# Kernel optimization log

Hardware: AMD Instinct MI355X
Metric: run time of the kernel (lower is better)

## Reference

```python
import jax, jax.numpy as jnp
import numpy as np
import math

H = 16          # num_heads
EPS = 1e-5      # LayerNorm eps (torch default)


def setup_inputs() -> dict:
    key = jax.random.key(0)
    ks = jax.random.split(key, 4)
    B, T, D = 2, 2048, 1024
    s = 1.0 / math.sqrt(D)
    return {
        "x": jax.random.normal(ks[0], (B, T, D), dtype=jnp.float32),
        "ln_g": jnp.ones((D,), jnp.float32),
        "ln_b": jnp.zeros((D,), jnp.float32),
        "Wq": jax.random.normal(ks[1], (D, D), jnp.float32) * s,
        "bq": jnp.zeros((D,), jnp.float32),
        "Wk": jax.random.normal(ks[2], (D, D), jnp.float32) * s,
        "bk": jnp.zeros((D,), jnp.float32),
        "Wv": jax.random.normal(ks[3], (D, D), jnp.float32) * s,
        "bv": jnp.zeros((D,), jnp.float32),
    }


def reference(x, ln_g, ln_b, Wq, bq, Wk, bk, Wv, bv):
    B, T, D = x.shape
    # LayerNorm (shared across the three projections, computed once)
    mu = jnp.mean(x, axis=-1, keepdims=True)
    var = jnp.mean(jnp.square(x - mu), axis=-1, keepdims=True)
    xn = (x - mu) * jax.lax.rsqrt(var + EPS) * ln_g + ln_b
    # Q/K/V projections -> [B, T, H, Dh]
    q = (xn @ Wq + bq).reshape(B, T, H, D // H)
    k = (xn @ Wk + bk).reshape(B, T, H, D // H)
    v = (xn @ Wv + bv).reshape(B, T, H, D // H)
    # QK^T scores [B, n, m, h], scaled by sqrt(head_dim)
    scale = 1.0 / math.sqrt(D // H)
    attn = jnp.einsum('bnhd,bmhd->bnmh', q, k) * scale
    # softmax over key axis (dim=2), dropout p=0 is identity
    w = jax.nn.softmax(attn, axis=2)
    # weighted sum of values, merge heads
    y = jnp.einsum('bnmh,bmhd->bnhd', w, v).reshape(B, T, D)
    return y
```

## Files before the change

### kernel.cpp

```cpp
#include <hip/hip_runtime.h>
#include <hip/hip_bf16.h>


typedef __attribute__((ext_vector_type(8)))  short short8;
typedef __attribute__((ext_vector_type(4)))  float f32x4;
typedef __attribute__((ext_vector_type(2)))  float f32x2;
typedef __attribute__((ext_vector_type(16))) float f32x16;
typedef __attribute__((ext_vector_type(2)))  unsigned int uint2v;

#define D_MODEL 1024
#define T_SEQ   2048
#define NHEAD   16
#define HDIM    64

#define LOG2E 1.4426950408889634f

#if defined(__has_builtin)
#if __has_builtin(__builtin_amdgcn_exp2f)
#define EXP2(x) __builtin_amdgcn_exp2f(x)
#endif
#if __has_builtin(__builtin_amdgcn_permlane32_swap)
#define HAVE_PERMSWAP 1
#endif
#endif
#ifndef EXP2
#define EXP2(x) exp2f(x)
#endif

__device__ __forceinline__ unsigned short f2bf(float x) {
    unsigned int u = __float_as_uint(x);
    u = (u + 0x7fffu + ((u >> 16) & 1u)) >> 16;
    return (unsigned short)u;
}

__device__ __forceinline__ uint2v permswap(unsigned a, unsigned b) {
#ifdef HAVE_PERMSWAP
    return __builtin_amdgcn_permlane32_swap(a, b, false, false);
#else
    uint2v r;
    const unsigned as = (unsigned)__shfl_xor((int)a, 32, 64);
    const unsigned bs = (unsigned)__shfl_xor((int)b, 32, 64);
    const bool hi = (threadIdx.x & 32) != 0;
    r[0] = hi ? bs : a;
    r[1] = hi ? b  : as;
    return r;
#endif
}

__device__ __forceinline__ void group_barrier() {
    asm volatile("s_waitcnt lgkmcnt(0)" ::: "memory");
    __builtin_amdgcn_s_barrier();
    asm volatile("" ::: "memory");
}

__device__ __forceinline__ void w8(unsigned short* p, const uint4 v) {
    uint2 a; a.x = v.x; a.y = v.y;
    uint2 b; b.x = v.z; b.y = v.w;
    *(uint2*)p = a;
    *(uint2*)(p + 4) = b;
}

__device__ __forceinline__ short8 read8(const unsigned short* p) {
    union { unsigned u[4]; short8 s; } r;
    const uint2 a = *(const uint2*)p;
    const uint2 b = *(const uint2*)(p + 4);
    r.u[0] = a.x; r.u[1] = a.y; r.u[2] = b.x; r.u[3] = b.y;
    return r.s;
}

__global__ __launch_bounds__(256) void ln_wcast_kernel(
    const float* __restrict__ x, const float* __restrict__ gam,
    const float* __restrict__ bet, unsigned short* __restrict__ xn,
    const float* __restrict__ Wq, const float* __restrict__ Wk,
    const float* __restrict__ Wv, unsigned short* __restrict__ Wt)
{
    __shared__ float red[8];
    __shared__ float tile[32][33];
    const int bid = blockIdx.x;
    if (bid < 4096) {
        const int row = bid;
        const int t = threadIdx.x;
        const float4 v = ((const float4*)(x + (size_t)row * D_MODEL))[t];
        float s  = v.x + v.y + v.z + v.w;
        float s2 = v.x * v.x + v.y * v.y + v.z * v.z + v.w * v.w;
#pragma unroll
        for (int off = 32; off; off >>= 1) {
            s  += __shfl_down(s,  off, 64);
            s2 += __shfl_down(s2, off, 64);
        }
        const int lane = t & 63, wave = t >> 6;
        if (lane == 0) { red[wave] = s; red[4 + wave] = s2; }
        __syncthreads();
        s  = red[0] + red[1] + red[2] + red[3];
        s2 = red[4] + red[5] + red[6] + red[7];
        const float mu   = s * (1.f / D_MODEL);
        const float var  = s2 * (1.f / D_MODEL) - mu * mu;
        const float rstd = rsqrtf(var + 1e-5f);
        const float4 gv = ((const float4*)gam)[t];
        const float4 bv = ((const float4*)bet)[t];
        ushort4 o;
        o.x = f2bf((v.x - mu) * rstd * gv.x + bv.x);
        o.y = f2bf((v.y - mu) * rstd * gv.y + bv.y);
        o.z = f2bf((v.z - mu) * rstd * gv.z + bv.z);
        o.w = f2bf((v.w - mu) * rstd * gv.w + bv.w);
        ((ushort4*)(xn + (size_t)row * D_MODEL))[t] = o;
    } else {
        const int id = bid - 4096;
        const int z  = id >> 10;
        const int t2 = id & 1023;
        const int n0 = (t2 & 31) * 32, k0 = (t2 >> 5) * 32;
        const float* W = (z == 0) ? Wq : (z == 1) ? Wk : Wv;
        unsigned short* outw = Wt + (size_t)z * D_MODEL * D_MODEL;
        const int tx = threadIdx.x & 31, ty = threadIdx.x >> 5;
#pragma unroll
        for (int i = ty; i < 32; i += 8)
            tile[i][tx] = W[(size_t)(k0 + i) * D_MODEL + n0 + tx];
        __syncthreads();
#pragma unroll
        for (int i = ty; i < 32; i += 8)
            outw[(size_t)(n0 + i) * D_MODEL + k0 + tx] = f2bf(tile[tx][i]);
    }
}

__global__ __launch_bounds__(256) void qkv_gemm_kernel(
    const unsigned short* __restrict__ xn, const unsigned short* __restrict__ Wt,
    const float* __restrict__ bq, const float* __restrict__ bk, const float* __restrict__ bv,
    unsigned short* __restrict__ qo, unsigned short* __restrict__ ko, unsigned short* __restrict__ vt)
{
    const int which = blockIdx.x >> 3;
    const int xt = blockIdx.x & 7, yt = blockIdx.y;
    const bool vmode = (which == 2);
    const unsigned short* Aptr = vmode ? (Wt + (size_t)2 * D_MODEL * D_MODEL) : xn;
    const unsigned short* Bptr = vmode ? xn : (Wt + (size_t)which * D_MODEL * D_MODEL);
    const float* bias   = (which == 0) ? bq : (which == 1) ? bk : bv;
    const float scale   = (which == 0) ? (0.125f * LOG2E) : 1.0f;
    const int m0 = vmode ? (yt & 15) * 64 : yt * 64;
    const int n0 = vmode ? (xt + (yt >> 4) * 8) * 128 : xt * 128;

    __shared__ unsigned short As[64][64];
    __shared__ unsigned short Bs[128][64];

    const int tid = threadIdx.x;
    const int lane = tid & 63, wave = tid >> 6;
    const int wc = wave;
    const int g = lane >> 4, c = lane & 15;

    const int srow = lane >> 3;
    const int swzc = (((lane & 7) * 8) ^ ((srow & 7) * 8));
    const int rsw  = (c & 7) * 8;

    f32x4 acc[4][2] = {};

    for (int kt = 0; kt < D_MODEL; kt += 64) {
        __syncthreads();
#pragma unroll
        for (int i = 0; i < 2; ++i) {
            const int r = wave * 16 + i * 8;
            const unsigned short* ga = Aptr + (size_t)(m0 + r + srow) * D_MODEL + kt + swzc;
            __builtin_amdgcn_global_load_lds(
                (const __attribute__((address_space(1))) unsigned int*)ga,
                (__attribute__((address_space(3))) unsigned int*)(&As[r][0]), 16, 0, 0);
        }
#pragma unroll
        for (int i = 0; i < 4; ++i) {
            const int r = wave * 32 + i * 8;
            const unsigned short* gb = Bptr + (size_t)(n0 + r + srow) * D_MODEL + kt + swzc;
            __builtin_amdgcn_global_load_lds(
                (const __attribute__((address_space(1))) unsigned int*)gb,
                (__attribute__((address_space(3))) unsigned int*)(&Bs[r][0]), 16, 0, 0);
        }
        __syncthreads();

        short8 af[4][2], bf[2][2];
#pragma unroll
        for (int i = 0; i < 4; ++i) {
            const int ra = i * 16 + c;
#pragma unroll
            for (int kk = 0; kk < 2; ++kk)
                af[i][kk] = *(const short8*)(&As[ra][(kk * 32 + g * 8) ^ rsw]);
        }
#pragma unroll
        for (int j = 0; j < 2; ++j) {
            const int rb = wc * 32 + j * 16 + c;
#pragma unroll
            for (int kk = 0; kk < 2; ++kk)
                bf[j][kk] = *(const short8*)(&Bs[rb][(kk * 32 + g * 8) ^ rsw]);
        }
#pragma unroll
        for (int kk = 0; kk < 2; ++kk)
#pragma unroll
            for (int i = 0; i < 4; ++i)
#pragma unroll
                for (int j = 0; j < 2; ++j)
                    acc[i][j] = __builtin_amdgcn_mfma_f32_16x16x32_bf16(
                        af[i][kk], bf[j][kk], acc[i][j], 0, 0, 0);
    }

    if (!vmode) {
        unsigned short* out = (which == 0) ? qo : ko;
#pragma unroll
        for (int j = 0; j < 2; ++j) {
            const int n = n0 + wc * 32 + j * 16 + c;
            const float bn = bias[n];
            const int h = n >> 6, dh = n & 63;
#pragma unroll
            for (int i = 0; i < 4; ++i) {
#pragma unroll
                for (int r = 0; r < 4; ++r) {
                    const int m = m0 + i * 16 + g * 4 + r;
                    const int bb = m >> 11, t = m & 2047;
                    out[((size_t)(bb * NHEAD + h) * T_SEQ + t) * HDIM + dh] =
                        f2bf((acc[i][j][r] + bn) * scale);
                }
            }
        }
    } else {
#pragma unroll
        for (int i = 0; i < 4; ++i) {
#pragma unroll
            for (int r = 0; r < 4; ++r) {
                const int m = m0 + i * 16 + g * 4 + r;
                const float bn = bias[m];
#pragma unroll
                for (int j = 0; j < 2; ++j) {
                    const int n = n0 + wc * 32 + j * 16 + c;
                    const int bb = n >> 11, t = n & 2047;
                    vt[(size_t)bb * (D_MODEL * T_SEQ) + (size_t)m * T_SEQ + t] =
                        f2bf(acc[i][j][r] + bn);
                }
            }
        }
    }
}

__global__ __launch_bounds__(512, 4) void attn_kernel(
    const unsigned short* __restrict__ qb, const unsigned short* __restrict__ kb,
    const unsigned short* __restrict__ vtb, float* __restrict__ out)
{
    const int id  = blockIdx.x;
    const int swz = (id & 7) * 64 + (id >> 3);
    const int qt  = swz & 15;
    const int bh  = swz >> 4;
    const int b = bh >> 4, head = bh & 15;
    const unsigned short* Q  = qb  + (size_t)bh * T_SEQ * HDIM;
    const unsigned short* Kp = kb  + (size_t)bh * T_SEQ * HDIM;
    const unsigned short* Vt = vtb + (size_t)b * (D_MODEL * T_SEQ)
                                   + (size_t)head * (HDIM * T_SEQ);

    __shared__ __align__(16) unsigned short smem[34816];

    const int tid = threadIdx.x, lane = tid & 63, wave = tid >> 6;
    const int grp = wave >> 2, w4 = wave & 3;
    const int q = lane & 31, h = lane >> 5;
    const int kvbase = grp * (T_SEQ / 2);

    const int gtid = tid & 255;
    const int sr = gtid >> 3;
    const int sc = (gtid & 7) * 8;

    unsigned short* gbase = &smem[grp * 17408];

    short8 qf[4];
    {
        const unsigned short* qp = Q + (size_t)(qt * 128 + w4 * 32 + q) * HDIM;
#pragma unroll
        for (int c = 0; c < 4; ++c)
            qf[c] = *(const short8*)(qp + c * 16 + h * 8);
    }

    float l_r = 0.f;
    f32x16 o[2] = {};

    const unsigned short* kp0 = Kp + (size_t)(kvbase + sr) * HDIM + sc;
    const unsigned short* vp0 = Vt + (size_t)sr * T_SEQ + kvbase + sc;
    uint4 kr0 = *(const uint4*)(kp0);
    uint4 kr1 = *(const uint4*)(kp0 + 32 * HDIM);
    uint4 vr0 = *(const uint4*)(vp0);
    uint4 vr1 = *(const uint4*)(vp0 + 32 * T_SEQ);
    w8(gbase + sr * 68 + sc, kr0);
    w8(gbase + (sr + 32) * 68 + sc, kr1);
    w8(gbase + 8704 + sr * 68 + sc, vr0);
    w8(gbase + 8704 + (sr + 32) * 68 + sc, vr1);
    kp0 += 64 * HDIM;
    vp0 += 64;

    int cur = 0;
#pragma unroll 1
    for (int t = 0; t < 16; ++t) {
        const bool more = (t + 1 < 16);
        if (more) {
            kr0 = *(const uint4*)(kp0);
            kr1 = *(const uint4*)(kp0 + 32 * HDIM);
            vr0 = *(const uint4*)(vp0);
            vr1 = *(const uint4*)(vp0 + 32 * T_SEQ);
            kp0 += 64 * HDIM;
            vp0 += 64;
        }
        group_barrier();
        const unsigned short* kbuf = gbase + cur * 4352;
        const unsigned short* vbuf = gbase + 8704 + cur * 4352;

        f32x16 s0 = {}, s1 = {};
        __builtin_amdgcn_s_setprio(1);
#pragma unroll
        for (int c = 0; c < 4; ++c) {
            const short8 kf0 = read8(kbuf + (size_t)q * 68 + c * 16 + h * 8);
            const short8 kf1 = read8(kbuf + (size_t)(32 + q) * 68 + c * 16 + h * 8);
            s0 = __builtin_amdgcn_mfma_f32_32x32x16_bf16(kf0, qf[c], s0, 0, 0, 0);
            s1 = __builtin_amdgcn_mfma_f32_32x32x16_bf16(kf1, qf[c], s1, 0, 0, 0);
        }
        __builtin_amdgcn_s_setprio(0);

#pragma unroll
        for (int r = 0; r < 16; ++r) { s0[r] = EXP2(s0[r]); }
#pragma unroll
        for (int r = 0; r < 16; ++r) { s1[r] = EXP2(s1[r]); }

        {
            f32x2 u[8];
#pragma unroll
            for (int r = 0; r < 8; ++r) {
                f32x2 a; a[0] = s0[2*r]; a[1] = s0[2*r+1];
                f32x2 bb; bb[0] = s1[2*r]; bb[1] = s1[2*r+1];
                u[r] = a + bb;
            }
            u[0] += u[1]; u[2] += u[3]; u[4] += u[5]; u[6] += u[7];
            u[0] += u[2]; u[4] += u[6];
            u[0] += u[4];
            float rs = u[0][0] + u[0][1];
            rs += __shfl_xor(rs, 32, 64);
            l_r += rs;
        }

        unsigned Wb0[8], Wb1[8];
#pragma unroll
        for (int u = 0; u < 4; ++u) {
            asm("v_cvt_pk_bf16_f32 %0, %1, %2" : "=v"(Wb0[u*2])   : "v"(s0[4*u]),   "v"(s0[4*u+1]));
            asm("v_cvt_pk_bf16_f32 %0, %1, %2" : "=v"(Wb0[u*2+1]) : "v"(s0[4*u+2]), "v"(s0[4*u+3]));
            asm("v_cvt_pk_bf16_f32 %0, %1, %2" : "=v"(Wb1[u*2])   : "v"(s1[4*u]),   "v"(s1[4*u+1]));
            asm("v_cvt_pk_bf16_f32 %0, %1, %2" : "=v"(Wb1[u*2+1]) : "v"(s1[4*u+2]), "v"(s1[4*u+3]));
        }

        short8 pf[4];
#pragma unroll
        for (int m = 0; m < 2; ++m) {
            {
                const uint2v r0 = permswap(Wb0[4*m],     Wb0[4*m + 2]);
                const uint2v r1 = permswap(Wb0[4*m + 1], Wb0[4*m + 3]);
                union { unsigned u[4]; short8 s; } pw;
                pw.u[0] = r0[0]; pw.u[1] = r1[0]; pw.u[2] = r0[1]; pw.u[3] = r1[1];
                pf[m] = pw.s;
            }
            {
                const uint2v r0 = permswap(Wb1[4*m],     Wb1[4*m + 2]);
                const uint2v r1 = permswap(Wb1[4*m + 1], Wb1[4*m + 3]);
                union { unsigned u[4]; short8 s; } pw;
                pw.u[0] = r0[0]; pw.u[1] = r1[0]; pw.u[2] = r0[1]; pw.u[3] = r1[1];
                pf[2 + m] = pw.s;
            }
        }

        __builtin_amdgcn_s_setprio(1);
#pragma unroll
        for (int dt = 0; dt < 2; ++dt) {
#pragma unroll
            for (int cp = 0; cp < 4; ++cp) {
                const short8 vf = read8(vbuf + (size_t)(dt * 32 + q) * 68 + cp * 16 + h * 8);
                o[dt] = __builtin_amdgcn_mfma_f32_32x32x16_bf16(vf, pf[cp], o[dt], 0, 0, 0);
            }
        }
        __builtin_amdgcn_s_setprio(0);

        if (more) {
            unsigned short* kd = gbase + (cur ^ 1) * 4352;
            unsigned short* vd = gbase + 8704 + (cur ^ 1) * 4352;
            w8(kd + sr * 68 + sc, kr0);
            w8(kd + (sr + 32) * 68 + sc, kr1);
            w8(vd + sr * 68 + sc, vr0);
            w8(vd + (sr + 32) * 68 + sc, vr1);
        }
        cur ^= 1;
    }

    __syncthreads();
    float* obuf  = (float*)(void*)smem;
    float* l_lds = ((float*)(void*)smem) + 128 * 68;

    const int qrl = w4 * 32 + q;
    if (grp == 0) {
#pragma unroll
        for (int dt = 0; dt < 2; ++dt)
#pragma unroll
            for (int u = 0; u < 4; ++u) {
                float* dst = obuf + (size_t)qrl * 68 + dt * 32 + 8 * u + 4 * h;
                float2 lo; lo.x = o[dt][4*u];     lo.y = o[dt][4*u + 1];
                float2 hi; hi.x = o[dt][4*u + 2]; hi.y = o[dt][4*u + 3];
                *(float2*)dst = lo;
                *(float2*)(dst + 2) = hi;
            }
        if (h == 0) l_lds[qrl] = l_r;
    }
    __syncthreads();
    if (grp == 1) {
        const float invl = 1.0f / (l_lds[qrl] + l_r);
#pragma unroll
        for (int dt = 0; dt < 2; ++dt)
#pragma unroll
            for (int u = 0; u < 4; ++u) {
                float* dst = obuf + (size_t)qrl * 68 + dt * 32 + 8 * u + 4 * h;
                float2 lo = *(const float2*)dst;
                float2 hi = *(const float2*)(dst + 2);
                lo.x = (lo.x + o[dt][4*u])     * invl;
                lo.y = (lo.y + o[dt][4*u + 1]) * invl;
                hi.x = (hi.x + o[dt][4*u + 2]) * invl;
                hi.y = (hi.y + o[dt][4*u + 3]) * invl;
                *(float2*)dst = lo;
                *(float2*)(dst + 2) = hi;
            }
    }
    __syncthreads();
#pragma unroll
    for (int it = 0; it < 4; ++it) {
        const int row = it * 32 + (tid >> 4);
        const int col = (tid & 15) * 4;
        const float4 v = *(const float4*)(&obuf[(size_t)row * 68 + col]);
        *(float4*)(&out[(size_t)(b * T_SEQ + qt * 128 + row) * D_MODEL + head * HDIM + col]) = v;
    }
}

extern "C" void kernel_launch(void* const* d_in, const int* in_sizes, int n_in,
                              void* d_out, int out_size, void* d_ws, size_t ws_size,
                              hipStream_t stream)
{
    const float* x   = (const float*)d_in[0];
    const float* lng = (const float*)d_in[1];
    const float* lnb = (const float*)d_in[2];
    const float* Wq  = (const float*)d_in[3];
    const float* bq  = (const float*)d_in[4];
    const float* Wk  = (const float*)d_in[5];
    const float* bk  = (const float*)d_in[6];
    const float* Wv  = (const float*)d_in[7];
    const float* bv  = (const float*)d_in[8];
    float* out = (float*)d_out;

    unsigned short* xn = (unsigned short*)d_ws;
    unsigned short* Wt = xn + (size_t)4096 * 1024;
    unsigned short* qh = Wt + (size_t)3 * 1024 * 1024;
    unsigned short* kh = qh + (size_t)4096 * 1024;
    unsigned short* vt = kh + (size_t)4096 * 1024;

    ln_wcast_kernel<<<7168, 256, 0, stream>>>(x, lng, lnb, xn, Wq, Wk, Wv, Wt);
    qkv_gemm_kernel<<<dim3(24, 64), 256, 0, stream>>>(xn, Wt, bq, bk, bv, qh, kh, vt);
    attn_kernel<<<512, 512, 0, stream>>>(qh, kh, vt, out);
}
```

Baseline: 91.14 us.

## Give each attention wave a private K/V staging buffer, removing block barriers

The attention kernel moves from 512-thread blocks with two shared, double-buffered K/V tiles per group to 256-thread blocks. Each wave now stages its own 32-key K and V tile in private LDS and loops over 32 smaller steps. This removes the per-iteration workgroup barrier, and the grid doubles to 1024 blocks of 64 query rows. In exchange each wave loads its K/V data redundantly, the per-wave tile is single-buffered with loads interleaved into compute, and the setprio hints are dropped.

Measured after the change: 111.9 us. 1.23x slower.

```diff
diff --git a/kernel.cpp b/kernel.cpp
--- a/kernel.cpp
+++ b/kernel.cpp
@@ -45,12 +45,6 @@
     r[1] = hi ? b  : as;
     return r;
 #endif
-}
-
-__device__ __forceinline__ void group_barrier() {
-    asm volatile("s_waitcnt lgkmcnt(0)" ::: "memory");
-    __builtin_amdgcn_s_barrier();
-    asm volatile("" ::: "memory");
 }
 
 __device__ __forceinline__ void w8(unsigned short* p, const uint4 v) {
@@ -233,36 +227,36 @@
     }
 }
 
-__global__ __launch_bounds__(512, 4) void attn_kernel(
+__global__ __launch_bounds__(256, 4) void attn_kernel(
     const unsigned short* __restrict__ qb, const unsigned short* __restrict__ kb,
     const unsigned short* __restrict__ vtb, float* __restrict__ out)
 {
     const int id  = blockIdx.x;
-    const int swz = (id & 7) * 64 + (id >> 3);
-    const int qt  = swz & 15;
-    const int bh  = swz >> 4;
+    const int swz = (id & 7) * 128 + (id >> 3);
+    const int qt  = swz & 31;
+    const int bh  = swz >> 5;
     const int b = bh >> 4, head = bh & 15;
     const unsigned short* Q  = qb  + (size_t)bh * T_SEQ * HDIM;
     const unsigned short* Kp = kb  + (size_t)bh * T_SEQ * HDIM;
     const unsigned short* Vt = vtb + (size_t)b * (D_MODEL * T_SEQ)
                                    + (size_t)head * (HDIM * T_SEQ);
 
-    __shared__ __align__(16) unsigned short smem[34816];
+    __shared__ __align__(16) unsigned short smem[17920];
 
     const int tid = threadIdx.x, lane = tid & 63, wave = tid >> 6;
-    const int grp = wave >> 2, w4 = wave & 3;
+    const int w2 = wave & 1, kvh = wave >> 1;
     const int q = lane & 31, h = lane >> 5;
-    const int kvbase = grp * (T_SEQ / 2);
-
-    const int gtid = tid & 255;
-    const int sr = gtid >> 3;
-    const int sc = (gtid & 7) * 8;
-
-    unsigned short* gbase = &smem[grp * 17408];
+    const int kvbase = kvh * (T_SEQ / 2);
+
+    unsigned short* kbuf = &smem[wave * 4480];
+    unsigned short* vbuf = kbuf + 2176;
+
+    const int krow = lane >> 3, kch = (lane & 7) * 8;
+    const int vrow = lane >> 2, vch = (lane & 3) * 8;
 
     short8 qf[4];
     {
-        const unsigned short* qp = Q + (size_t)(qt * 128 + w4 * 32 + q) * HDIM;
+        const unsigned short* qp = Q + (size_t)(qt * 64 + w2 * 32 + q) * HDIM;
 #pragma unroll
         for (int c = 0; c < 4; ++c)
             qf[c] = *(const short8*)(qp + c * 16 + h * 8);
@@ -271,59 +265,46 @@
     float l_r = 0.f;
     f32x16 o[2] = {};
 
-    const unsigned short* kp0 = Kp + (size_t)(kvbase + sr) * HDIM + sc;
-    const unsigned short* vp0 = Vt + (size_t)sr * T_SEQ + kvbase + sc;
-    uint4 kr0 = *(const uint4*)(kp0);
-    uint4 kr1 = *(const uint4*)(kp0 + 32 * HDIM);
-    uint4 vr0 = *(const uint4*)(vp0);
-    uint4 vr1 = *(const uint4*)(vp0 + 32 * T_SEQ);
-    w8(gbase + sr * 68 + sc, kr0);
-    w8(gbase + (sr + 32) * 68 + sc, kr1);
-    w8(gbase + 8704 + sr * 68 + sc, vr0);
-    w8(gbase + 8704 + (sr + 32) * 68 + sc, vr1);
-    kp0 += 64 * HDIM;
-    vp0 += 64;
-
-    int cur = 0;
+    {
+        const unsigned short* kp = Kp + (size_t)(kvbase + krow) * HDIM + kch;
+        const unsigned short* vp = Vt + (size_t)vrow * T_SEQ + kvbase + vch;
+        uint4 kr[4], vr[4];
+#pragma unroll
+        for (int i = 0; i < 4; ++i) kr[i] = *(const uint4*)(kp + (size_t)i * 8 * HDIM);
+#pragma unroll
+        for (int i = 0; i < 4; ++i) vr[i] = *(const uint4*)(vp + (size_t)i * 16 * T_SEQ);
+#pragma unroll
+        for (int i = 0; i < 4; ++i) w8(kbuf + (i * 8 + krow) * 68 + kch, kr[i]);
+#pragma unroll
+        for (int i = 0; i < 4; ++i) w8(vbuf + (i * 16 + vrow) * 36 + vch, vr[i]);
+    }
+
 #pragma unroll 1
-    for (int t = 0; t < 16; ++t) {
-        const bool more = (t + 1 < 16);
+    for (int t = 0; t < 32; ++t) {
+        const bool more = (t + 1 < 32);
+        const int kvn = kvbase + (t + 1) * 32;
+
+        uint4 kr[4];
         if (more) {
-            kr0 = *(const uint4*)(kp0);
-            kr1 = *(const uint4*)(kp0 + 32 * HDIM);
-            vr0 = *(const uint4*)(vp0);
-            vr1 = *(const uint4*)(vp0 + 32 * T_SEQ);
-            kp0 += 64 * HDIM;
-            vp0 += 64;
-        }
-        group_barrier();
-        const unsigned short* kbuf = gbase + cur * 4352;
-        const unsigned short* vbuf = gbase + 8704 + cur * 4352;
-
-        f32x16 s0 = {}, s1 = {};
-        __builtin_amdgcn_s_setprio(1);
+            const unsigned short* kp = Kp + (size_t)(kvn + krow) * HDIM + kch;
+#pragma unroll
+            for (int i = 0; i < 4; ++i) kr[i] = *(const uint4*)(kp + (size_t)i * 8 * HDIM);
+        }
+
+        f32x16 s = {};
 #pragma unroll
         for (int c = 0; c < 4; ++c) {
-            const short8 kf0 = read8(kbuf + (size_t)q * 68 + c * 16 + h * 8);
-            const short8 kf1 = read8(kbuf + (size_t)(32 + q) * 68 + c * 16 + h * 8);
-            s0 = __builtin_amdgcn_mfma_f32_32x32x16_bf16(kf0, qf[c], s0, 0, 0, 0);
-            s1 = __builtin_amdgcn_mfma_f32_32x32x16_bf16(kf1, qf[c], s1, 0, 0, 0);
-        }
-        __builtin_amdgcn_s_setprio(0);
-
-#pragma unroll
-        for (int r = 0; r < 16; ++r) { s0[r] = EXP2(s0[r]); }
-#pragma unroll
-        for (int r = 0; r < 16; ++r) { s1[r] = EXP2(s1[r]); }
+            const short8 kf = read8(kbuf + (size_t)q * 68 + c * 16 + h * 8);
+            s = __builtin_amdgcn_mfma_f32_32x32x16_bf16(kf, qf[c], s, 0, 0, 0);
+        }
+
+#pragma unroll
+        for (int r = 0; r < 16; ++r) { s[r] = EXP2(s[r]); }
 
         {
             f32x2 u[8];
 #pragma unroll
-            for (int r = 0; r < 8; ++r) {
-                f32x2 a; a[0] = s0[2*r]; a[1] = s0[2*r+1];
-                f32x2 bb; bb[0] = s1[2*r]; bb[1] = s1[2*r+1];
-                u[r] = a + bb;
-            }
+            for (int r = 0; r < 8; ++r) { f32x2 a; a[0] = s[2*r]; a[1] = s[2*r+1]; u[r] = a; }
             u[0] += u[1]; u[2] += u[3]; u[4] += u[5]; u[6] += u[7];
             u[0] += u[2]; u[4] += u[6];
             u[0] += u[4];
@@ -332,62 +313,55 @@
             l_r += rs;
         }
 
-        unsigned Wb0[8], Wb1[8];
+        unsigned Wb[8];
 #pragma unroll
         for (int u = 0; u < 4; ++u) {
-            asm("v_cvt_pk_bf16_f32 %0, %1, %2" : "=v"(Wb0[u*2])   : "v"(s0[4*u]),   "v"(s0[4*u+1]));
-            asm("v_cvt_pk_bf16_f32 %0, %1, %2" : "=v"(Wb0[u*2+1]) : "v"(s0[4*u+2]), "v"(s0[4*u+3]));
-            asm("v_cvt_pk_bf16_f32 %0, %1, %2" : "=v"(Wb1[u*2])   : "v"(s1[4*u]),   "v"(s1[4*u+1]));
-            asm("v_cvt_pk_bf16_f32 %0, %1, %2" : "=v"(Wb1[u*2+1]) : "v"(s1[4*u+2]), "v"(s1[4*u+3]));
-        }
-
-        short8 pf[4];
+            asm("v_cvt_pk_bf16_f32 %0, %1, %2" : "=v"(Wb[u*2])   : "v"(s[4*u]),   "v"(s[4*u+1]));
+            asm("v_cvt_pk_bf16_f32 %0, %1, %2" : "=v"(Wb[u*2+1]) : "v"(s[4*u+2]), "v"(s[4*u+3]));
+        }
+
+        short8 pf[2];
 #pragma unroll
         for (int m = 0; m < 2; ++m) {
-            {
-                const uint2v r0 = permswap(Wb0[4*m],     Wb0[4*m + 2]);
-                const uint2v r1 = permswap(Wb0[4*m + 1], Wb0[4*m + 3]);
-                union { unsigned u[4]; short8 s; } pw;
-                pw.u[0] = r0[0]; pw.u[1] = r1[0]; pw.u[2] = r0[1]; pw.u[3] = r1[1];
-                pf[m] = pw.s;
+            const uint2v r0 = permswap(Wb[4*m],     Wb[4*m + 2]);
+            const uint2v r1 = permswap(Wb[4*m + 1], Wb[4*m + 3]);
+            union { unsigned u[4]; short8 s; } pw;
+            pw.u[0] = r0[0]; pw.u[1] = r1[0]; pw.u[2] = r0[1]; pw.u[3] = r1[1];
+            pf[m] = pw.s;
+        }
+
+        if (more) {
+#pragma unroll
+            for (int i = 0; i < 4; ++i) w8(kbuf + (i * 8 + krow) * 68 + kch, kr[i]);
+        }
+        uint4 vr[4];
+        if (more) {
+            const unsigned short* vp = Vt + (size_t)vrow * T_SEQ + kvn + vch;
+#pragma unroll
+            for (int i = 0; i < 4; ++i) vr[i] = *(const uint4*)(vp + (size_t)i * 16 * T_SEQ);
+        }
+
+#pragma unroll
+        for (int dt = 0; dt < 2; ++dt) {
+#pragma unroll
+            for (int kk = 0; kk < 2; ++kk) {
+                const short8 vf = read8(vbuf + (size_t)(dt * 32 + q) * 36 + kk * 16 + h * 8);
+                o[dt] = __builtin_amdgcn_mfma_f32_32x32x16_bf16(vf, pf[kk], o[dt], 0, 0, 0);
             }
-            {
-                const uint2v r0 = permswap(Wb1[4*m],     Wb1[4*m + 2]);
-                const uint2v r1 = permswap(Wb1[4*m + 1], Wb1[4*m + 3]);
-                union { unsigned u[4]; short8 s; } pw;
-                pw.u[0] = r0[0]; pw.u[1] = r1[0]; pw.u[2] = r0[1]; pw.u[3] = r1[1];
-                pf[2 + m] = pw.s;
-            }
-        }
-
-        __builtin_amdgcn_s_setprio(1);
-#pragma unroll
-        for (int dt = 0; dt < 2; ++dt) {
-#pragma unroll
-            for (int cp = 0; cp < 4; ++cp) {
-                const short8 vf = read8(vbuf + (size_t)(dt * 32 + q) * 68 + cp * 16 + h * 8);
-                o[dt] = __builtin_amdgcn_mfma_f32_32x32x16_bf16(vf, pf[cp], o[dt], 0, 0, 0);
-            }
-        }
-        __builtin_amdgcn_s_setprio(0);
+        }
 
         if (more) {
-            unsigned short* kd = gbase + (cur ^ 1) * 4352;
-            unsigned short* vd = gbase + 8704 + (cur ^ 1) * 4352;
-            w8(kd + sr * 68 + sc, kr0);
-            w8(kd + (sr + 32) * 68 + sc, kr1);
-            w8(vd + sr * 68 + sc, vr0);
-            w8(vd + (sr + 32) * 68 + sc, vr1);
-        }
-        cur ^= 1;
+#pragma unroll
+            for (int i = 0; i < 4; ++i) w8(vbuf + (i * 16 + vrow) * 36 + vch, vr[i]);
+        }
     }
 
     __syncthreads();
     float* obuf  = (float*)(void*)smem;
-    float* l_lds = ((float*)(void*)smem) + 128 * 68;
-
-    const int qrl = w4 * 32 + q;
-    if (grp == 0) {
+    float* l_lds = ((float*)(void*)smem) + 64 * 68;
+
+    const int qrl = w2 * 32 + q;
+    if (kvh == 0) {
 #pragma unroll
         for (int dt = 0; dt < 2; ++dt)
 #pragma unroll
@@ -401,7 +375,7 @@
         if (h == 0) l_lds[qrl] = l_r;
     }
     __syncthreads();
-    if (grp == 1) {
+    if (kvh == 1) {
         const float invl = 1.0f / (l_lds[qrl] + l_r);
 #pragma unroll
         for (int dt = 0; dt < 2; ++dt)
@@ -420,11 +394,14 @@
     }
     __syncthreads();
 #pragma unroll
-    for (int it = 0; it < 4; ++it) {
-        const int row = it * 32 + (tid >> 4);
-        const int col = (tid & 15) * 4;
-        const float4 v = *(const float4*)(&obuf[(size_t)row * 68 + col]);
-        *(float4*)(&out[(size_t)(b * T_SEQ + qt * 128 + row) * D_MODEL + head * HDIM + col]) = v;
+    for (int it = 0; it < 2; ++it) {
+        const int row = it * 32 + (tid >> 3);
+        const int col = (tid & 7) * 8;
+        const float4 v0 = *(const float4*)(&obuf[(size_t)row * 68 + col]);
+        const float4 v1 = *(const float4*)(&obuf[(size_t)row * 68 + col + 4]);
+        float* op = &out[(size_t)(b * T_SEQ + qt * 64 + row) * D_MODEL + head * HDIM + col];
+        *(float4*)op = v0;
+        *(float4*)(op + 4) = v1;
     }
 }
 
@@ -451,5 +428,5 @@
 
     ln_wcast_kernel<<<7168, 256, 0, stream>>>(x, lng, lnb, xn, Wq, Wk, Wv, Wt);
     qkv_gemm_kernel<<<dim3(24, 64), 256, 0, stream>>>(xn, Wt, bq, bk, bv, qh, kh, vt);
-    attn_kernel<<<512, 512, 0, stream>>>(qh, kh, vt, out);
-}
+    attn_kernel<<<1024, 256, 0, stream>>>(qh, kh, vt, out);
+}
```
